# Optimization experiments

Hardware: AMD Instinct MI355X
Metric: run time of the kernel (lower is better)

Reference implementation:

```python
import jax, jax.numpy as jnp
import numpy as np

B, N, T, E = 8, 1024, 16, 512
H = 8                      # heads
DH = E // H                # head_dim = 64
KNN = 16                   # knn_k (N-1 > 16 so k = 16)
L = 4                      # time_window (<= T)
TAU_MIN = 1e-4
BIAS_SCALE = 1.0


def setup_inputs() -> dict:
    key = jax.random.key(0)
    ks = jax.random.split(key, 12)
    hidden = jax.random.normal(ks[0], (B, N, T, E), jnp.float32)
    positions_xy = jax.random.uniform(ks[1], (N, 2), jnp.float32) * 100.0
    s = 1.0 / np.sqrt(E)
    Wq = jax.random.normal(ks[2], (E, E), jnp.float32) * s
    bq = jnp.zeros((E,), jnp.float32)
    Wk = jax.random.normal(ks[3], (E, E), jnp.float32) * s
    bk = jnp.zeros((E,), jnp.float32)
    Wv = jax.random.normal(ks[4], (E, E), jnp.float32) * s
    bv = jnp.zeros((E,), jnp.float32)
    Wo = jax.random.normal(ks[5], (E, E), jnp.float32) * s
    bo = jnp.zeros((E,), jnp.float32)
    tau = jnp.asarray(1.0, jnp.float32)
    return {"hidden": hidden, "positions_xy": positions_xy,
            "Wq": Wq, "bq": bq, "Wk": Wk, "bk": bk,
            "Wv": Wv, "bv": bv, "Wo": Wo, "bo": bo, "tau": tau}


def reference(hidden, positions_xy, Wq, bq, Wk, bk, Wv, bv, Wo, bo, tau):
    b, n, t, e = hidden.shape
    # --- kNN over static positions (no_grad in the original) ---
    pos = jax.lax.stop_gradient(positions_xy)
    x2 = jnp.sum(pos * pos, axis=1, keepdims=True)          # [N,1]
    d2 = jnp.clip(x2 + x2.T - 2.0 * (pos @ pos.T), 0.0)
    D = jnp.sqrt(d2 + 1e-9)
    D = D + jnp.diag(jnp.full((n,), jnp.inf, D.dtype))       # exclude self
    neg_d, knn_idx = jax.lax.top_k(-D, KNN)                  # smallest-k
    knn_dists = -neg_d                                        # [N,K]

    h_last = hidden[:, :, -1, :]                              # [B,N,E]
    # mean over last L steps, then gather neighbors (== gather-then-mean)
    neigh_mean = jnp.mean(hidden[:, :, -L:, :], axis=2)       # [B,N,E]
    neigh_repr = neigh_mean[:, knn_idx]                       # [B,N,K,E]

    # --- distance bias ---
    eps = jnp.finfo(hidden.dtype).eps
    local_scale = jnp.maximum(jnp.mean(knn_dists, axis=1, keepdims=True), eps)
    d_hat = knn_dists / local_scale                           # [N,K]
    tau_safe = jnp.maximum(tau, TAU_MIN)
    log_w = jnp.clip(BIAS_SCALE * (-d_hat / tau_safe), -10.0, 0.0)

    # --- distance-biased multi-head attention over k neighbors ---
    Q = (h_last @ Wq.T + bq).reshape(b, n, H, DH)             # [B,N,H,Dh]
    K = (neigh_repr @ Wk.T + bk).reshape(b, n, KNN, H, DH)    # [B,N,K,H,Dh]
    V = (neigh_repr @ Wv.T + bv).reshape(b, n, KNN, H, DH)
    logits = jnp.einsum('bnhd,bnkhd->bnhk', Q, K) / jnp.sqrt(jnp.asarray(DH, hidden.dtype))
    logits = logits + log_w[None, :, None, :]                 # [B,N,H,K]
    attn = jax.nn.softmax(logits, axis=-1)                    # dropout=0 (eval)
    ctx = jnp.einsum('bnhk,bnkhd->bnhd', attn, V).reshape(b, n, H * DH)
    return ctx @ Wo.T + bo                                    # [B,N,E]
```

## Files before the change

kernel.cpp:

```cpp
#include <hip/hip_runtime.h>
#include <math.h>

#define B_   8
#define N_   1024
#define T_   16
#define E_   512
#define H_   8
#define DH_  64
#define KNN_ 16

typedef __attribute__((ext_vector_type(8))) _Float16 half8;
typedef __attribute__((ext_vector_type(4))) float    f32x4;

__global__ __launch_bounds__(256) void knn_kernel(const float* __restrict__ pos,
                                                  const float* __restrict__ tau_p,
                                                  int* __restrict__ knn_idx,
                                                  float* __restrict__ logw) {
    __shared__ float dist[N_];
    __shared__ float rval[4];
    __shared__ int   ridx[4];
    __shared__ float sel_d[KNN_];
    __shared__ int   sel_i[KNN_];

    const int i = blockIdx.x;
    const int t = threadIdx.x;

    const float px = pos[2 * i], py = pos[2 * i + 1];
    const float xi2 = px * px + py * py;

    for (int j = t; j < N_; j += 256) {
        const float qx = pos[2 * j], qy = pos[2 * j + 1];
        const float xj2 = qx * qx + qy * qy;
        float d2 = xi2 + xj2 - 2.0f * (px * qx + py * qy);
        d2 = fmaxf(d2, 0.0f);
        const float d = sqrtf(d2 + 1e-9f);
        dist[j] = (j == i) ? __builtin_inff() : d;
    }
    __syncthreads();

    for (int k = 0; k < KNN_; ++k) {
        float best = __builtin_inff();
        int bi = 0x7fffffff;
        for (int j = t; j < N_; j += 256) {
            const float d = dist[j];
            if (d < best) { best = d; bi = j; }
        }
        for (int off = 32; off >= 1; off >>= 1) {
            const float ov = __shfl_down(best, off);
            const int   oi = __shfl_down(bi, off);
            if (ov < best || (ov == best && oi < bi)) { best = ov; bi = oi; }
        }
        const int wave = t >> 6;
        if ((t & 63) == 0) { rval[wave] = best; ridx[wave] = bi; }
        __syncthreads();
        if (t == 0) {
            for (int w = 1; w < 4; ++w) {
                if (rval[w] < best || (rval[w] == best && ridx[w] < bi)) { best = rval[w]; bi = ridx[w]; }
            }
            sel_d[k] = best;
            sel_i[k] = bi;
            dist[bi] = __builtin_inff();
        }
        __syncthreads();
    }

    if (t < KNN_) {
        float mean = 0.0f;
        for (int k = 0; k < KNN_; ++k) mean += sel_d[k];
        mean *= (1.0f / KNN_);
        const float scale = fmaxf(mean, 1.1920929e-7f);
        const float tau_safe = fmaxf(tau_p[0], 1e-4f);
        float lw = -(sel_d[t] / scale) / tau_safe;
        lw = fminf(fmaxf(lw, -10.0f), 0.0f);
        logw[i * KNN_ + t]    = lw;
        knn_idx[i * KNN_ + t] = sel_i[t];
    }
}

__global__ __launch_bounds__(256) void last_mean_kernel(const float* __restrict__ hidden,
                                                        float* __restrict__ h_last,
                                                        float* __restrict__ neigh_mean) {
    const int idx = blockIdx.x * 256 + threadIdx.x;
    const int e4 = idx & (E_ / 4 - 1);
    const int bn = idx >> 7;
    const float4* h = (const float4*)hidden;
    const size_t base = (size_t)bn * (T_ * (E_ / 4)) + e4;
    const float4 a = h[base + 12 * (E_ / 4)];
    const float4 b = h[base + 13 * (E_ / 4)];
    const float4 c = h[base + 14 * (E_ / 4)];
    const float4 d = h[base + 15 * (E_ / 4)];
    ((float4*)h_last)[idx] = d;
    float4 m;
    m.x = (a.x + b.x + c.x + d.x) * 0.25f;
    m.y = (a.y + b.y + c.y + d.y) * 0.25f;
    m.z = (a.z + b.z + c.z + d.z) * 0.25f;
    m.w = (a.w + b.w + c.w + d.w) * 0.25f;
    ((float4*)neigh_mean)[idx] = m;
}

__device__ __forceinline__ void split_store(unsigned short* __restrict__ Hs,
                                            unsigned short* __restrict__ Ls,
                                            int byt, float4 v) {
    union { _Float16 h[4]; uint2 u; } Hu, Lu;
    const float* f = (const float*)&v;
#pragma unroll
    for (int j = 0; j < 4; ++j) {
        const _Float16 hh = (_Float16)f[j];
        Hu.h[j] = hh;
        Lu.h[j] = (_Float16)(f[j] - (float)hh);
    }
    *(uint2*)((char*)Hs + byt) = Hu.u;
    *(uint2*)((char*)Ls + byt) = Lu.u;
}

__device__ __forceinline__ void gemm_split_f16(const float* __restrict__ A,
                                               const float* __restrict__ Wt,
                                               const float* __restrict__ bias,
                                               float* __restrict__ C) {
    __shared__ unsigned short AhS[128 * 64];
    __shared__ unsigned short AlS[128 * 64];
    __shared__ unsigned short WhS[128 * 64];
    __shared__ unsigned short WlS[128 * 64];

    const int t    = threadIdx.x;
    const int m0   = blockIdx.x * 128;
    const int j0   = blockIdx.y * 128;
    const int lane = t & 63;
    const int wv   = t >> 6;
    const int wm   = wv >> 1;
    const int wn   = wv & 1;
    const int lr   = lane & 15;
    const int kg   = lane >> 4;

    float4 ra[8], rw[8];
#pragma unroll
    for (int s = 0; s < 8; ++s) {
        const int f4 = s * 256 + t;
        const int row = f4 >> 4, k4 = f4 & 15;
        ra[s] = *(const float4*)(A  + (size_t)(m0 + row) * 512 + k4 * 4);
        rw[s] = *(const float4*)(Wt + (size_t)(j0 + row) * 512 + k4 * 4);
    }

    f32x4 acc[4][4];
    const f32x4 zero = {0.0f, 0.0f, 0.0f, 0.0f};
#pragma unroll
    for (int f = 0; f < 4; ++f)
#pragma unroll
        for (int g = 0; g < 4; ++g) acc[f][g] = zero;

    for (int it = 0; it < 8; ++it) {
        __syncthreads();
#pragma unroll
        for (int s = 0; s < 8; ++s) {
            const int f4 = s * 256 + t;
            const int row = f4 >> 4, k4 = f4 & 15;
            const int byt = (row << 7) + ((k4 * 8) ^ ((row & 7) << 4));
            split_store(AhS, AlS, byt, ra[s]);
            split_store(WhS, WlS, byt, rw[s]);
        }
        __syncthreads();
        if (it < 7) {
            const int kc = (it + 1) * 64;
#pragma unroll
            for (int s = 0; s < 8; ++s) {
                const int f4 = s * 256 + t;
                const int row = f4 >> 4, k4 = f4 & 15;
                ra[s] = *(const float4*)(A  + (size_t)(m0 + row) * 512 + kc + k4 * 4);
                rw[s] = *(const float4*)(Wt + (size_t)(j0 + row) * 512 + kc + k4 * 4);
            }
        }
#pragma unroll
        for (int ks = 0; ks < 2; ++ks) {
            half8 ah[4], al[4], wh[4], wl[4];
#pragma unroll
            for (int f = 0; f < 4; ++f) {
                const int row = wm * 64 + f * 16 + lr;
                const int byt = (row << 7) + (((ks * 64) + (kg * 16)) ^ ((row & 7) << 4));
                ah[f] = *(const half8*)((const char*)AhS + byt);
                al[f] = *(const half8*)((const char*)AlS + byt);
            }
#pragma unroll
            for (int g = 0; g < 4; ++g) {
                const int row = wn * 64 + g * 16 + lr;
                const int byt = (row << 7) + (((ks * 64) + (kg * 16)) ^ ((row & 7) << 4));
                wh[g] = *(const half8*)((const char*)WhS + byt);
                wl[g] = *(const half8*)((const char*)WlS + byt);
            }
#pragma unroll
            for (int f = 0; f < 4; ++f)
#pragma unroll
                for (int g = 0; g < 4; ++g)
                    acc[f][g] = __builtin_amdgcn_mfma_f32_16x16x32_f16(ah[f], wh[g], acc[f][g], 0, 0, 0);
#pragma unroll
            for (int f = 0; f < 4; ++f)
#pragma unroll
                for (int g = 0; g < 4; ++g)
                    acc[f][g] = __builtin_amdgcn_mfma_f32_16x16x32_f16(ah[f], wl[g], acc[f][g], 0, 0, 0);
#pragma unroll
            for (int f = 0; f < 4; ++f)
#pragma unroll
                for (int g = 0; g < 4; ++g)
                    acc[f][g] = __builtin_amdgcn_mfma_f32_16x16x32_f16(al[f], wh[g], acc[f][g], 0, 0, 0);
        }
    }

#pragma unroll
    for (int g = 0; g < 4; ++g) {
        const int n  = j0 + wn * 64 + g * 16 + lr;
        const float bn = bias[n];
#pragma unroll
        for (int f = 0; f < 4; ++f) {
            const int mrow = m0 + wm * 64 + f * 16 + kg * 4;
#pragma unroll
            for (int q = 0; q < 4; ++q)
                C[(size_t)(mrow + q) * 512 + n] = acc[f][g][q] + bn;
        }
    }
}

__global__ __launch_bounds__(256, 2) void qkv_gemm_kernel(const float* __restrict__ h_last,
                                                          const float* __restrict__ nmean,
                                                          const float* __restrict__ Wq,
                                                          const float* __restrict__ Wk,
                                                          const float* __restrict__ Wv,
                                                          const float* __restrict__ bq,
                                                          const float* __restrict__ bk,
                                                          const float* __restrict__ bv,
                                                          float* __restrict__ Qo,
                                                          float* __restrict__ Ko,
                                                          float* __restrict__ Vo) {
    const int which = blockIdx.z;
    const float* A    = (which == 0) ? h_last : nmean;
    const float* W    = (which == 0) ? Wq : (which == 1) ? Wk : Wv;
    const float* bias = (which == 0) ? bq : (which == 1) ? bk : bv;
    float*       C    = (which == 0) ? Qo : (which == 1) ? Ko : Vo;
    gemm_split_f16(A, W, bias, C);
}

__global__ __launch_bounds__(256, 2) void out_gemm_kernel(const float* __restrict__ ctx,
                                                          const float* __restrict__ Wo,
                                                          const float* __restrict__ bo,
                                                          float* __restrict__ out) {
    gemm_split_f16(ctx, Wo, bo, out);
}

__global__ __launch_bounds__(256) void attn_kernel(const float* __restrict__ Q,
                                                   const float* __restrict__ Kf,
                                                   const float* __restrict__ Vf,
                                                   const int* __restrict__ knn_idx,
                                                   const float* __restrict__ logw,
                                                   float* __restrict__ ctx) {
    const int bn = blockIdx.x;
    const int n  = bn & (N_ - 1);
    const int b  = bn >> 10;
    const int t  = threadIdx.x;

    __shared__ int   idxs[KNN_];
    __shared__ float lws[KNN_];
    if (t < KNN_) {
        idxs[t] = knn_idx[n * KNN_ + t];
        lws[t]  = logw[n * KNN_ + t];
    }
    __syncthreads();

    const float2 q = ((const float2*)Q)[(size_t)bn * 256 + t];

    float logits[KNN_];
#pragma unroll
    for (int k = 0; k < KNN_; ++k) {
        const int j = idxs[k];
        const float2 kv = ((const float2*)Kf)[((size_t)(b * N_ + j)) * 256 + t];
        float d = q.x * kv.x + q.y * kv.y;
        d += __shfl_xor(d, 1);
        d += __shfl_xor(d, 2);
        d += __shfl_xor(d, 4);
        d += __shfl_xor(d, 8);
        d += __shfl_xor(d, 16);
        logits[k] = d * 0.125f + lws[k];
    }

    float m = -__builtin_inff();
#pragma unroll
    for (int k = 0; k < KNN_; ++k) m = fmaxf(m, logits[k]);
    float p[KNN_];
    float s = 0.0f;
#pragma unroll
    for (int k = 0; k < KNN_; ++k) { p[k] = expf(logits[k] - m); s += p[k]; }
    const float inv = 1.0f / s;

    float2 acc = make_float2(0.0f, 0.0f);
#pragma unroll
    for (int k = 0; k < KNN_; ++k) {
        const int j = idxs[k];
        const float2 vv = ((const float2*)Vf)[((size_t)(b * N_ + j)) * 256 + t];
        const float w = p[k] * inv;
        acc.x = fmaf(w, vv.x, acc.x);
        acc.y = fmaf(w, vv.y, acc.y);
    }
    ((float2*)ctx)[(size_t)bn * 256 + t] = acc;
}

extern "C" void kernel_launch(void* const* d_in, const int* in_sizes, int n_in,
                              void* d_out, int out_size, void* d_ws, size_t ws_size,
                              hipStream_t stream) {
    const float* hidden = (const float*)d_in[0];
    const float* pos    = (const float*)d_in[1];
    const float* Wq     = (const float*)d_in[2];
    const float* bq     = (const float*)d_in[3];
    const float* Wk     = (const float*)d_in[4];
    const float* bk     = (const float*)d_in[5];
    const float* Wv     = (const float*)d_in[6];
    const float* bv     = (const float*)d_in[7];
    const float* Wo     = (const float*)d_in[8];
    const float* bo     = (const float*)d_in[9];
    const float* tau    = (const float*)d_in[10];

    float* ws      = (float*)d_ws;
    const size_t SZ = (size_t)B_ * N_ * E_;
    float* h_last  = ws;
    float* nmean   = ws + SZ;
    float* Kb      = ws + 2 * SZ;
    float* Vb      = ws + 3 * SZ;
    int*   knn_idx = (int*)(ws + 4 * SZ);
    float* logw    = ws + 4 * SZ + N_ * KNN_;
    float* Qb      = (float*)d_out;
    float* out     = (float*)d_out;

    knn_kernel<<<N_, 256, 0, stream>>>(pos, tau, knn_idx, logw);
    last_mean_kernel<<<(B_ * N_ * E_ / 4) / 256, 256, 0, stream>>>(hidden, h_last, nmean);

    dim3 gqkv(B_ * N_ / 128, E_ / 128, 3);
    qkv_gemm_kernel<<<gqkv, 256, 0, stream>>>(h_last, nmean, Wq, Wk, Wv, bq, bk, bv, Qb, Kb, Vb);

    attn_kernel<<<B_ * N_, 256, 0, stream>>>(Qb, Kb, Vb, knn_idx, logw, h_last );

    dim3 gout(B_ * N_ / 128, E_ / 128, 1);
    out_gemm_kernel<<<gout, 256, 0, stream>>>(h_last, Wo, bo, out);
}
```

Measured before the change: 474.3 us.

## Store K/V projections in fp16 and remap attention blocks across batches

The QKV GEMM now writes the K and V projections as fp16 instead of fp32. This halves their write traffic and halves the gather traffic in the attention kernel, which dequantizes the values to float on load. The attention kernel's block index is also remapped to interleave batches, changing the order in which the gathered neighbor rows are reused across concurrently running blocks. Storing K and V in fp16 loses precision relative to the split-fp16 GEMM's roughly fp32 accuracy, which risks a larger numerical error.

```diff
diff --git a/kernel.cpp b/kernel.cpp
--- a/kernel.cpp
+++ b/kernel.cpp
@@ -10,6 +10,7 @@
 #define KNN_ 16
 
 typedef __attribute__((ext_vector_type(8))) _Float16 half8;
+typedef __attribute__((ext_vector_type(2))) _Float16 half2v;
 typedef __attribute__((ext_vector_type(4))) float    f32x4;
 
 __global__ __launch_bounds__(256) void knn_kernel(const float* __restrict__ pos,
@@ -113,10 +114,11 @@
     *(uint2*)((char*)Ls + byt) = Lu.u;
 }
 
+template <typename OT>
 __device__ __forceinline__ void gemm_split_f16(const float* __restrict__ A,
                                                const float* __restrict__ Wt,
                                                const float* __restrict__ bias,
-                                               float* __restrict__ C) {
+                                               OT* __restrict__ C) {
     __shared__ unsigned short AhS[128 * 64];
     __shared__ unsigned short AlS[128 * 64];
     __shared__ unsigned short WhS[128 * 64];
@@ -213,7 +215,7 @@
             const int mrow = m0 + wm * 64 + f * 16 + kg * 4;
 #pragma unroll
             for (int q = 0; q < 4; ++q)
-                C[(size_t)(mrow + q) * 512 + n] = acc[f][g][q] + bn;
+                C[(size_t)(mrow + q) * 512 + n] = (OT)(acc[f][g][q] + bn);
         }
     }
 }
@@ -227,33 +229,36 @@
                                                           const float* __restrict__ bk,
                                                           const float* __restrict__ bv,
                                                           float* __restrict__ Qo,
-                                                          float* __restrict__ Ko,
-                                                          float* __restrict__ Vo) {
+                                                          _Float16* __restrict__ Ko,
+                                                          _Float16* __restrict__ Vo) {
     const int which = blockIdx.z;
-    const float* A    = (which == 0) ? h_last : nmean;
-    const float* W    = (which == 0) ? Wq : (which == 1) ? Wk : Wv;
-    const float* bias = (which == 0) ? bq : (which == 1) ? bk : bv;
-    float*       C    = (which == 0) ? Qo : (which == 1) ? Ko : Vo;
-    gemm_split_f16(A, W, bias, C);
+    if (which == 0) {
+        gemm_split_f16<float>(h_last, Wq, bq, Qo);
+    } else if (which == 1) {
+        gemm_split_f16<_Float16>(nmean, Wk, bk, Ko);
+    } else {
+        gemm_split_f16<_Float16>(nmean, Wv, bv, Vo);
+    }
 }
 
 __global__ __launch_bounds__(256, 2) void out_gemm_kernel(const float* __restrict__ ctx,
                                                           const float* __restrict__ Wo,
                                                           const float* __restrict__ bo,
                                                           float* __restrict__ out) {
-    gemm_split_f16(ctx, Wo, bo, out);
+    gemm_split_f16<float>(ctx, Wo, bo, out);
 }
 
 __global__ __launch_bounds__(256) void attn_kernel(const float* __restrict__ Q,
-                                                   const float* __restrict__ Kf,
-                                                   const float* __restrict__ Vf,
+                                                   const _Float16* __restrict__ Kf,
+                                                   const _Float16* __restrict__ Vf,
                                                    const int* __restrict__ knn_idx,
                                                    const float* __restrict__ logw,
                                                    float* __restrict__ ctx) {
-    const int bn = blockIdx.x;
-    const int n  = bn & (N_ - 1);
-    const int b  = bn >> 10;
-    const int t  = threadIdx.x;
+    const int bid = blockIdx.x;
+    const int bn  = ((bid & 7) << 10) | (bid >> 3);
+    const int n   = bn & (N_ - 1);
+    const int b   = bn >> 10;
+    const int t   = threadIdx.x;
 
     __shared__ int   idxs[KNN_];
     __shared__ float lws[KNN_];
@@ -269,8 +274,8 @@
 #pragma unroll
     for (int k = 0; k < KNN_; ++k) {
         const int j = idxs[k];
-        const float2 kv = ((const float2*)Kf)[((size_t)(b * N_ + j)) * 256 + t];
-        float d = q.x * kv.x + q.y * kv.y;
+        const half2v kv = ((const half2v*)Kf)[((size_t)(b * N_ + j)) * 256 + t];
+        float d = q.x * (float)kv.x + q.y * (float)kv.y;
         d += __shfl_xor(d, 1);
         d += __shfl_xor(d, 2);
         d += __shfl_xor(d, 4);
@@ -292,10 +297,10 @@
 #pragma unroll
     for (int k = 0; k < KNN_; ++k) {
         const int j = idxs[k];
-        const float2 vv = ((const float2*)Vf)[((size_t)(b * N_ + j)) * 256 + t];
+        const half2v vv = ((const half2v*)Vf)[((size_t)(b * N_ + j)) * 256 + t];
         const float w = p[k] * inv;
-        acc.x = fmaf(w, vv.x, acc.x);
-        acc.y = fmaf(w, vv.y, acc.y);
+        acc.x = fmaf(w, (float)vv.x, acc.x);
+        acc.y = fmaf(w, (float)vv.y, acc.y);
     }
     ((float2*)ctx)[(size_t)bn * 256 + t] = acc;
 }
@@ -317,22 +322,22 @@
 
     float* ws      = (float*)d_ws;
     const size_t SZ = (size_t)B_ * N_ * E_;
-    float* h_last  = ws;
-    float* nmean   = ws + SZ;
-    float* Kb      = ws + 2 * SZ;
-    float* Vb      = ws + 3 * SZ;
-    int*   knn_idx = (int*)(ws + 4 * SZ);
-    float* logw    = ws + 4 * SZ + N_ * KNN_;
-    float* Qb      = (float*)d_out;
-    float* out     = (float*)d_out;
+    float*    h_last  = ws;
+    float*    nmean   = ws + SZ;
+    _Float16* Kh      = (_Float16*)(ws + 2 * SZ);
+    _Float16* Vh      = (_Float16*)(ws + 2 * SZ + SZ / 2);
+    int*      knn_idx = (int*)(ws + 3 * SZ);
+    float*    logw    = ws + 3 * SZ + N_ * KNN_;
+    float*    Qb      = (float*)d_out;
+    float*    out     = (float*)d_out;
 
     knn_kernel<<<N_, 256, 0, stream>>>(pos, tau, knn_idx, logw);
     last_mean_kernel<<<(B_ * N_ * E_ / 4) / 256, 256, 0, stream>>>(hidden, h_last, nmean);
 
     dim3 gqkv(B_ * N_ / 128, E_ / 128, 3);
-    qkv_gemm_kernel<<<gqkv, 256, 0, stream>>>(h_last, nmean, Wq, Wk, Wv, bq, bk, bv, Qb, Kb, Vb);
-
-    attn_kernel<<<B_ * N_, 256, 0, stream>>>(Qb, Kb, Vb, knn_idx, logw, h_last );
+    qkv_gemm_kernel<<<gqkv, 256, 0, stream>>>(h_last, nmean, Wq, Wk, Wv, bq, bk, bv, Qb, Kh, Vh);
+
+    attn_kernel<<<B_ * N_, 256, 0, stream>>>(Qb, Kh, Vh, knn_idx, logw, h_last );
 
     dim3 gout(B_ * N_ / 128, E_ / 128, 1);
     out_gemm_kernel<<<gout, 256, 0, stream>>>(h_last, Wo, bo, out);
```

Measured after the change: 478.9 us. About the same (+1.0%).
